# Kernel tuning notes

Measured on AMD Instinct MI355X. Metric: run time of the kernel, lower is better.

Reference implementation:

```python
import jax, jax.numpy as jnp
import numpy as np

B, L, CIN, COUT, HEADS = 8, 2048, 256, 256, 4
HD = COUT // HEADS
NEG_SLOPE = 0.2


def setup_inputs() -> dict:
    key = jax.random.key(0)
    k1, k2, k3, k4, k5 = jax.random.split(key, 5)
    x = jax.random.normal(k1, (B, L, CIN), dtype=jnp.float32)
    adj_mask = jax.random.randint(k2, (B, L, L), 0, 2) > 0  # bool [B,L,L]
    W = jax.random.normal(k3, (COUT, CIN), dtype=jnp.float32) * (1.0 / np.sqrt(CIN))
    att_src = jax.random.normal(k4, (1, HEADS, 1, HD), dtype=jnp.float32) * 0.1
    att_dst = jax.random.normal(k5, (1, HEADS, 1, HD), dtype=jnp.float32) * 0.1
    return {"x": x, "adj_mask": adj_mask, "W": W, "att_src": att_src, "att_dst": att_dst}


def reference(x, adj_mask, W, att_src, att_dst):
    Bb, Ll, _ = x.shape
    # linear projection (no bias), split heads: [B, H, L, D]
    h = jnp.einsum('blc,oc->blo', x, W).reshape(Bb, Ll, HEADS, HD).transpose(0, 2, 1, 3)
    # additive GAT scores
    a_src = jnp.sum(h * att_src, axis=-1, keepdims=True)          # [B,H,L,1]
    a_dst = jnp.sum(h * att_dst, axis=-1, keepdims=True)          # [B,H,L,1]
    e = a_src + jnp.swapaxes(a_dst, 2, 3)                          # [B,H,L,L]
    e = jnp.where(e >= 0, e, NEG_SLOPE * e)                        # leaky relu
    fill = jnp.finfo(e.dtype).min
    e = jnp.where(adj_mask[:, None, :, :], e, fill)                # mask non-edges
    alpha = jax.nn.softmax(e, axis=-1)                             # [B,H,L,L]
    # dropout is identity in eval/reference mode
    out = jnp.einsum('bhij,bhjd->bhid', alpha, h)                  # [B,H,L,D]
    return out.transpose(0, 2, 1, 3).reshape(Bb, Ll, COUT)
```

## Files before the change

kernel.cpp:

```cpp
#include <hip/hip_runtime.h>

#define B_ 8
#define L_ 2048
#define CIN_ 256
#define COUT_ 256
#define HEADS_ 4
#define HD_ 64
#define NEG_SLOPE_ 0.2f

#define TI 32
#define TJ 64
#define NJT (L_ / TJ)

typedef __attribute__((ext_vector_type(4))) float f32x4;
typedef __attribute__((ext_vector_type(8))) __bf16 bf16x8;
typedef __attribute__((ext_vector_type(4))) __bf16 bf16x4;


__global__ __launch_bounds__(256, 4)
void pack_kernel(const int* __restrict__ adj, unsigned long long* __restrict__ abits) {
  const size_t wid = ((size_t)blockIdx.x * 256 + threadIdx.x) >> 6;
  const int lane = threadIdx.x & 63;
  const int* p = adj + wid * 256 + lane;
  unsigned long long b0 = __ballot(p[0]   != 0);
  unsigned long long b1 = __ballot(p[64]  != 0);
  unsigned long long b2 = __ballot(p[128] != 0);
  unsigned long long b3 = __ballot(p[192] != 0);
  if (lane == 0) {
    ulonglong2 v01; v01.x = b0; v01.y = b1;
    ulonglong2 v23; v23.x = b2; v23.y = b3;
    *(ulonglong2*)(abits + wid * 4)     = v01;
    *(ulonglong2*)(abits + wid * 4 + 2) = v23;
  }
}

__global__ __launch_bounds__(256, 2)
void proj_kernel(const float* __restrict__ x, const float* __restrict__ W,
                 const float* __restrict__ att_src, const float* __restrict__ att_dst,
                 __bf16* __restrict__ hF, float* __restrict__ a_src,
                 float* __restrict__ a_dst) {
  __shared__ __align__(16) __bf16 Wl[COUT_][80];
  __shared__ __align__(16) __bf16 Al[2][2][512];

  const int tid = threadIdx.x;
  const int r0 = blockIdx.x * TI;
  const int b  = r0 >> 11;
  const int l0 = r0 & (L_ - 1);

  const int w = tid >> 6, lane = tid & 63, col = lane & 15, q = lane >> 4;
  const int si = tid >> 3, soct = tid & 7;
  const int wn = tid >> 2, wkq = tid & 3;

  f32x4 acc[2][4];
#pragma unroll
  for (int mt = 0; mt < 2; ++mt)
#pragma unroll
    for (int nt = 0; nt < 4; ++nt) acc[mt][nt] = (f32x4)0.f;

  for (int kc = 0; kc < CIN_ / 64; ++kc) {
    __syncthreads();
#pragma unroll
    for (int rg = 0; rg < 4; ++rg) {
      const int row = rg * 64 + wn;
      const float4* ws = (const float4*)(W + (size_t)row * CIN_ + kc * 64 + wkq * 16);
#pragma unroll
      for (int u = 0; u < 4; ++u) {
        float4 f = ws[u];
        bf16x4 v;
        v[0] = (__bf16)f.x; v[1] = (__bf16)f.y; v[2] = (__bf16)f.z; v[3] = (__bf16)f.w;
        *(bf16x4*)&Wl[row][wkq * 16 + u * 4] = v;
      }
    }
    {
      const float4* xs = (const float4*)(x + (size_t)(r0 + si) * CIN_ + kc * 64 + soct * 8);
      float4 f0 = xs[0], f1 = xs[1];
      bf16x8 v;
      v[0] = (__bf16)f0.x; v[1] = (__bf16)f0.y; v[2] = (__bf16)f0.z; v[3] = (__bf16)f0.w;
      v[4] = (__bf16)f1.x; v[5] = (__bf16)f1.y; v[6] = (__bf16)f1.z; v[7] = (__bf16)f1.w;
      *(bf16x8*)&Al[si >> 4][soct >> 2][(((soct & 3) << 4) + (si & 15)) << 3] = v;
    }
    __syncthreads();

    bf16x8 af[2][2], bfr[2][4];
#pragma unroll
    for (int mt = 0; mt < 2; ++mt)
#pragma unroll
      for (int kt = 0; kt < 2; ++kt)
        af[mt][kt] = *(const bf16x8*)&Al[mt][kt][lane << 3];
#pragma unroll
    for (int kt = 0; kt < 2; ++kt)
#pragma unroll
      for (int nt = 0; nt < 4; ++nt)
        bfr[kt][nt] = *(const bf16x8*)&Wl[w * 64 + nt * 16 + col][kt * 32 + q * 8];
#pragma unroll
    for (int kt = 0; kt < 2; ++kt)
#pragma unroll
      for (int mt = 0; mt < 2; ++mt)
#pragma unroll
        for (int nt = 0; nt < 4; ++nt)
          acc[mt][nt] = __builtin_amdgcn_mfma_f32_16x16x32_bf16(
              af[mt][kt], bfr[kt][nt], acc[mt][nt], 0, 0, 0);
  }

  float asv[4], adv[4];
#pragma unroll
  for (int nt = 0; nt < 4; ++nt) {
    asv[nt] = att_src[w * 64 + nt * 16 + col];
    adv[nt] = att_dst[w * 64 + nt * 16 + col];
  }
#pragma unroll
  for (int mt = 0; mt < 2; ++mt)
#pragma unroll
    for (int reg = 0; reg < 4; ++reg) {
      float s = 0.f, d = 0.f;
#pragma unroll
      for (int nt = 0; nt < 4; ++nt) {
        s = fmaf(acc[mt][nt][reg], asv[nt], s);
        d = fmaf(acc[mt][nt][reg], adv[nt], d);
      }
      s += __shfl_xor(s, 1, 64); d += __shfl_xor(d, 1, 64);
      s += __shfl_xor(s, 2, 64); d += __shfl_xor(d, 2, 64);
      s += __shfl_xor(s, 4, 64); d += __shfl_xor(d, 4, 64);
      s += __shfl_xor(s, 8, 64); d += __shfl_xor(d, 8, 64);
      if (col == 0) {
        int il = mt * 16 + q * 4 + reg;
        a_src[((size_t)(b * HEADS_ + w) << 11) + l0 + il] = s;
        a_dst[((size_t)(b * HEADS_ + w) << 11) + l0 + il] = d;
      }
    }

  {
    const int jt_p = l0 >> 6;
    const int kt_p = (l0 >> 5) & 1;
    const int qhi = q >> 1, qlo = q & 1;
#pragma unroll
    for (int mt = 0; mt < 2; ++mt) {
      const int qp = mt * 2 + qhi;
#pragma unroll
      for (int nt = 0; nt < 4; ++nt) {
        bf16x4 v;
        v[0] = (__bf16)acc[mt][nt][0];
        v[1] = (__bf16)acc[mt][nt][1];
        v[2] = (__bf16)acc[mt][nt][2];
        v[3] = (__bf16)acc[mt][nt][3];
        const size_t off =
            ((((size_t)(b * HEADS_ + w) * 32 + jt_p) * 2 + kt_p) * 4 + nt) * 512 +
            (qp * 16 + col) * 8 + qlo * 4;
        *(bf16x4*)(hF + off) = v;
      }
    }
  }
}

__global__ __launch_bounds__(256, 2)
void attn_kernel(const __bf16* __restrict__ hF, const float* __restrict__ a_src,
                 const float* __restrict__ a_dst,
                 const unsigned long long* __restrict__ abits,
                 float* __restrict__ out) {
  const int tid = threadIdx.x;
  const int b  = blockIdx.x & 7;
  const int i0 = (blockIdx.x >> 3) * 32;

  const int w = tid >> 6, lane = tid & 63, col = lane & 15, q = lane >> 4;

  const size_t hl = (size_t)(b * HEADS_ + w);
  const float asr[2] = {a_src[(hl << 11) + i0 + col],
                        a_src[(hl << 11) + i0 + 16 + col]};
  const float* adb = a_dst + (hl << 11) + q * 8;
  const __bf16* hb = hF + hl * 131072 + lane * 8;
  const unsigned long long* bp0 = abits + (((size_t)b << 11) + i0 + col) * 32;
  const unsigned long long* bp1 = bp0 + (16 * 32);

  f32x4 acc[2][4];
#pragma unroll
  for (int mt = 0; mt < 2; ++mt)
#pragma unroll
    for (int nt = 0; nt < 4; ++nt) acc[mt][nt] = (f32x4)0.f;
  float lacc[2] = {0.f, 0.f};

  bf16x8 cb[2][4];
  float4 cd[2][2];
  unsigned long long cw0, cw1;
#pragma unroll
  for (int kt = 0; kt < 2; ++kt) {
#pragma unroll
    for (int nt = 0; nt < 4; ++nt)
      cb[kt][nt] = *(const bf16x8*)(hb + (kt * 4 + nt) * 512);
    cd[kt][0] = *(const float4*)(adb + kt * 32);
    cd[kt][1] = *(const float4*)(adb + kt * 32 + 4);
  }
  cw0 = bp0[0];
  cw1 = bp1[0];

#pragma unroll 2
  for (int jt = 0; jt < NJT; ++jt) {
    const int jn = (jt < NJT - 1) ? jt + 1 : jt;

    bf16x8 nb[2][4];
    float4 nd[2][2];
#pragma unroll
    for (int kt = 0; kt < 2; ++kt) {
#pragma unroll
      for (int nt = 0; nt < 4; ++nt)
        nb[kt][nt] = *(const bf16x8*)(hb + jn * 4096 + (kt * 4 + nt) * 512);
      nd[kt][0] = *(const float4*)(adb + jn * 64 + kt * 32);
      nd[kt][1] = *(const float4*)(adb + jn * 64 + kt * 32 + 4);
    }
    const unsigned long long nw0 = bp0[jn];
    const unsigned long long nw1 = bp1[jn];

    bf16x8 av[2][2];
#pragma unroll
    for (int mt = 0; mt < 2; ++mt) {
      const unsigned long long bw = mt ? cw1 : cw0;
#pragma unroll
      for (int kt = 0; kt < 2; ++kt) {
        const unsigned int tsh = ((unsigned int)(bw >> (kt * 32))) >> (q * 8);
        const float dd[8] = {cd[kt][0].x, cd[kt][0].y, cd[kt][0].z, cd[kt][0].w,
                             cd[kt][1].x, cd[kt][1].y, cd[kt][1].z, cd[kt][1].w};
        float ls = 0.f;
#pragma unroll
        for (int e = 0; e < 8; ++e) {
          float s = asr[mt] + dd[e];
          s = fmaxf(s, NEG_SLOPE_ * s);
          float p = ((tsh >> e) & 1u) ? __expf(s) : 0.f;
          ls += p;
          av[mt][kt][e] = (__bf16)p;
        }
        lacc[mt] += ls;
      }
    }

#pragma unroll
    for (int kt = 0; kt < 2; ++kt)
#pragma unroll
      for (int mt = 0; mt < 2; ++mt)
#pragma unroll
        for (int nt = 0; nt < 4; ++nt)
          acc[mt][nt] = __builtin_amdgcn_mfma_f32_16x16x32_bf16(
              av[mt][kt], cb[kt][nt], acc[mt][nt], 0, 0, 0);

#pragma unroll
    for (int kt = 0; kt < 2; ++kt) {
#pragma unroll
      for (int nt = 0; nt < 4; ++nt) cb[kt][nt] = nb[kt][nt];
      cd[kt][0] = nd[kt][0];
      cd[kt][1] = nd[kt][1];
    }
    cw0 = nw0;
    cw1 = nw1;
  }

#pragma unroll
  for (int mt = 0; mt < 2; ++mt) {
    lacc[mt] += __shfl_xor(lacc[mt], 16, 64);
    lacc[mt] += __shfl_xor(lacc[mt], 32, 64);
  }

#pragma unroll
  for (int mt = 0; mt < 2; ++mt)
#pragma unroll
    for (int reg = 0; reg < 4; ++reg) {
      const int m = q * 4 + reg;
      const float linv = 1.0f / __shfl(lacc[mt], m, 64);
      const size_t orow =
          ((size_t)(b * L_ + i0 + mt * 16 + m)) * COUT_ + w * 64;
#pragma unroll
      for (int nt = 0; nt < 4; ++nt)
        out[orow + nt * 16 + col] = acc[mt][nt][reg] * linv;
    }
}

extern "C" void kernel_launch(void* const* d_in, const int* in_sizes, int n_in,
                              void* d_out, int out_size, void* d_ws, size_t ws_size,
                              hipStream_t stream) {
  const float* x       = (const float*)d_in[0];
  const int*   adj     = (const int*)d_in[1];
  const float* W       = (const float*)d_in[2];
  const float* att_src = (const float*)d_in[3];
  const float* att_dst = (const float*)d_in[4];
  float* out = (float*)d_out;

  char* ws = (char*)d_ws;
  __bf16* hF = (__bf16*)ws;
  float* a_src = (float*)(ws + (8u << 20));
  float* a_dst = (float*)(ws + (8u << 20) + (256u << 10));
  unsigned long long* abits =
      (unsigned long long*)(ws + (8u << 20) + (512u << 10));

  pack_kernel<<<(B_ * L_ * (L_ / 256)) / 4, 256, 0, stream>>>(adj, abits);
  proj_kernel<<<(B_ * L_) / TI, 256, 0, stream>>>(x, W, att_src, att_dst, hF, a_src, a_dst);
  attn_kernel<<<B_ * (L_ / 32), 256, 0, stream>>>(hF, a_src, a_dst, abits, out);
}
```

Baseline: 267.3 us.

## Drop register prefetch, raise occupancy, and fold log2e into scores for exp2

Removes the explicit next-tile register double-buffering in the attention loop and raises launch bounds from 2 to 4 blocks per CU. The aim is to hide memory latency through more resident waves instead of prefetched registers. Pre-scales a_src/a_dst by log2(e) in the projection kernel so the inner loop can call exp2 directly, which is valid because leaky ReLU commutes with positive scaling. MFMAs are also interleaved per row tile right after its probabilities are computed. The risk is exposed load latency if the extra occupancy does not cover it, or register spills under the tighter limit.

```diff
diff --git a/kernel.cpp b/kernel.cpp
--- a/kernel.cpp
+++ b/kernel.cpp
@@ -7,6 +7,7 @@
 #define HEADS_ 4
 #define HD_ 64
 #define NEG_SLOPE_ 0.2f
+#define LOG2E_ 1.4426950408889634f
 
 #define TI 32
 #define TJ 64
@@ -124,8 +125,8 @@
       s += __shfl_xor(s, 8, 64); d += __shfl_xor(d, 8, 64);
       if (col == 0) {
         int il = mt * 16 + q * 4 + reg;
-        a_src[((size_t)(b * HEADS_ + w) << 11) + l0 + il] = s;
-        a_dst[((size_t)(b * HEADS_ + w) << 11) + l0 + il] = d;
+        a_src[((size_t)(b * HEADS_ + w) << 11) + l0 + il] = s * LOG2E_;
+        a_dst[((size_t)(b * HEADS_ + w) << 11) + l0 + il] = d * LOG2E_;
       }
     }
 
@@ -152,7 +153,7 @@
   }
 }
 
-__global__ __launch_bounds__(256, 2)
+__global__ __launch_bounds__(256, 4)
 void attn_kernel(const __bf16* __restrict__ hF, const float* __restrict__ a_src,
                  const float* __restrict__ a_dst,
                  const unsigned long long* __restrict__ abits,
@@ -178,77 +179,47 @@
     for (int nt = 0; nt < 4; ++nt) acc[mt][nt] = (f32x4)0.f;
   float lacc[2] = {0.f, 0.f};
 
-  bf16x8 cb[2][4];
-  float4 cd[2][2];
-  unsigned long long cw0, cw1;
-#pragma unroll
-  for (int kt = 0; kt < 2; ++kt) {
-#pragma unroll
-    for (int nt = 0; nt < 4; ++nt)
-      cb[kt][nt] = *(const bf16x8*)(hb + (kt * 4 + nt) * 512);
-    cd[kt][0] = *(const float4*)(adb + kt * 32);
-    cd[kt][1] = *(const float4*)(adb + kt * 32 + 4);
-  }
-  cw0 = bp0[0];
-  cw1 = bp1[0];
-
-#pragma unroll 2
   for (int jt = 0; jt < NJT; ++jt) {
-    const int jn = (jt < NJT - 1) ? jt + 1 : jt;
-
-    bf16x8 nb[2][4];
-    float4 nd[2][2];
+    bf16x8 cb[2][4];
+#pragma unroll
+    for (int kt = 0; kt < 2; ++kt)
+#pragma unroll
+      for (int nt = 0; nt < 4; ++nt)
+        cb[kt][nt] = *(const bf16x8*)(hb + jt * 4096 + (kt * 4 + nt) * 512);
+    float4 cd[2][2];
 #pragma unroll
     for (int kt = 0; kt < 2; ++kt) {
-#pragma unroll
-      for (int nt = 0; nt < 4; ++nt)
-        nb[kt][nt] = *(const bf16x8*)(hb + jn * 4096 + (kt * 4 + nt) * 512);
-      nd[kt][0] = *(const float4*)(adb + jn * 64 + kt * 32);
-      nd[kt][1] = *(const float4*)(adb + jn * 64 + kt * 32 + 4);
-    }
-    const unsigned long long nw0 = bp0[jn];
-    const unsigned long long nw1 = bp1[jn];
-
-    bf16x8 av[2][2];
+      cd[kt][0] = *(const float4*)(adb + jt * 64 + kt * 32);
+      cd[kt][1] = *(const float4*)(adb + jt * 64 + kt * 32 + 4);
+    }
+    const unsigned long long cw[2] = {bp0[jt], bp1[jt]};
+
 #pragma unroll
     for (int mt = 0; mt < 2; ++mt) {
-      const unsigned long long bw = mt ? cw1 : cw0;
+      bf16x8 av[2];
 #pragma unroll
       for (int kt = 0; kt < 2; ++kt) {
-        const unsigned int tsh = ((unsigned int)(bw >> (kt * 32))) >> (q * 8);
+        const unsigned int tsh = ((unsigned int)(cw[mt] >> (kt * 32))) >> (q * 8);
         const float dd[8] = {cd[kt][0].x, cd[kt][0].y, cd[kt][0].z, cd[kt][0].w,
                              cd[kt][1].x, cd[kt][1].y, cd[kt][1].z, cd[kt][1].w};
         float ls = 0.f;
 #pragma unroll
         for (int e = 0; e < 8; ++e) {
-          float s = asr[mt] + dd[e];
-          s = fmaxf(s, NEG_SLOPE_ * s);
-          float p = ((tsh >> e) & 1u) ? __expf(s) : 0.f;
+          float t = asr[mt] + dd[e];
+          t = fmaxf(t, NEG_SLOPE_ * t);
+          float p = ((tsh >> e) & 1u) ? __builtin_exp2f(t) : 0.f;
           ls += p;
-          av[mt][kt][e] = (__bf16)p;
+          av[kt][e] = (__bf16)p;
         }
         lacc[mt] += ls;
       }
-    }
-
-#pragma unroll
-    for (int kt = 0; kt < 2; ++kt)
-#pragma unroll
-      for (int mt = 0; mt < 2; ++mt)
+#pragma unroll
+      for (int kt = 0; kt < 2; ++kt)
 #pragma unroll
         for (int nt = 0; nt < 4; ++nt)
           acc[mt][nt] = __builtin_amdgcn_mfma_f32_16x16x32_bf16(
-              av[mt][kt], cb[kt][nt], acc[mt][nt], 0, 0, 0);
-
-#pragma unroll
-    for (int kt = 0; kt < 2; ++kt) {
-#pragma unroll
-      for (int nt = 0; nt < 4; ++nt) cb[kt][nt] = nb[kt][nt];
-      cd[kt][0] = nd[kt][0];
-      cd[kt][1] = nd[kt][1];
-    }
-    cw0 = nw0;
-    cw1 = nw1;
+              av[kt], cb[kt][nt], acc[mt][nt], 0, 0, 0);
+    }
   }
 
 #pragma unroll
```

Result: slower. 283.1 us (+5.9%).
